# Optimization experiments

Hardware: AMD Instinct MI355X
Metric: run time of the kernel (lower is better)

The kernel has to match this reference:

```python
import jax, jax.numpy as jnp
import numpy as np

N, D_IN, HID, OUT, E = 131072, 256, 1024, 1, 100


def setup_inputs() -> dict:
    key = jax.random.key(0)
    k = jax.random.split(key, 7)
    return {
        "x": jax.random.normal(k[0], (N, D_IN), dtype=jnp.float32),
        "W1": jax.random.normal(k[1], (HID, D_IN), dtype=jnp.float32) * 0.05,
        "b1": jax.random.normal(k[2], (HID,), dtype=jnp.float32) * 0.05,
        "We": jax.random.normal(k[3], (E, OUT, HID), dtype=jnp.float32) * 0.05,
        "be": jax.random.normal(k[4], (E, OUT), dtype=jnp.float32) * 0.05,
        "num": jax.random.randint(k[5], (N,), 0, E, dtype=jnp.int64),
        "c": jax.random.randint(k[6], (E,), 0, E, dtype=jnp.int64),
    }


def reference(x, W1, b1, We, be, num, c):
    # feature: Linear + ReLU  -> [N, HID]
    h = jax.nn.relu(x @ W1.T + b1)
    # per-sample expert index: c[num[i]]
    e = c[num]                                  # [N]
    Wg = We[e]                                  # [N, OUT, HID] gathered expert weights
    bg = be[e]                                  # [N, OUT]
    y = jnp.einsum('noh,nh->no', Wg, h) + bg    # per-sample expert linear
    return jax.nn.sigmoid(y)
```

## Files before the change

kernel.cpp:

```cpp
#include <hip/hip_runtime.h>
#include <stdint.h>

#define N_SAMP 131072
#define DIN    256
#define HIDN   1024
#define BROWS  128
#define NTHREADS 256
#define NCHUNK 16

typedef __attribute__((ext_vector_type(8))) short short8;
typedef __attribute__((ext_vector_type(4))) float f32x4;

__device__ __forceinline__ unsigned short f2bf(float f) {
  unsigned u = __float_as_uint(f);
  u += 0x7fffu + ((u >> 16) & 1u);
  return (unsigned short)(u >> 16);
}

__device__ __forceinline__ short8 pack8(float4 a, float4 b) {
  short8 r;
  r[0] = (short)f2bf(a.x); r[1] = (short)f2bf(a.y);
  r[2] = (short)f2bf(a.z); r[3] = (short)f2bf(a.w);
  r[4] = (short)f2bf(b.x); r[5] = (short)f2bf(b.y);
  r[6] = (short)f2bf(b.z); r[7] = (short)f2bf(b.w);
  return r;
}

__global__ __launch_bounds__(256) void w1_pack(const float* __restrict__ W1,
                                               unsigned short* __restrict__ o) {
  int idx = blockIdx.x * 256 + threadIdx.x;
  int l  = idx & 63;
  int nt = (idx >> 6) & 3;
  int s  = (idx >> 8) & 7;
  int ch = idx >> 11;
  int col = ch * 64 + nt * 16 + (l & 15);
  int k0  = s * 32 + (l >> 4) * 8;
  const float* src = W1 + (size_t)col * DIN + k0;
  float4 f0 = *(const float4*)src;
  float4 f1 = *(const float4*)(src + 4);
  ((short8*)o)[idx] = pack8(f0, f1);
}

template <bool WBF>
__global__ __launch_bounds__(NTHREADS, 2) void fused_kernel(
    const float* __restrict__ x,
    const float* __restrict__ W1f,
    const unsigned short* __restrict__ W1p,
    const float* __restrict__ b1,
    const float* __restrict__ We,
    const float* __restrict__ be,
    const int* __restrict__ num,
    const int* __restrict__ c,
    float* __restrict__ out)
{
  __shared__ int e_sh[BROWS];

  const int tid  = threadIdx.x;
  const int lane = tid & 63;
  const int w    = tid >> 6;
  const int n    = lane & 15;
  const int quad = lane >> 4;
  const int R0   = blockIdx.x * BROWS;

  if (tid < BROWS) e_sh[tid] = c[num[R0 + tid]];

  short8 afr[2][8];
  {
    const float* xr0 = x + (size_t)(R0 + w * 32 + n) * DIN + quad * 8;
#pragma unroll
    for (int t = 0; t < 2; ++t) {
      const float* xr = xr0 + (size_t)t * 16 * DIN;
#pragma unroll
      for (int s = 0; s < 8; ++s) {
        float4 f0 = *(const float4*)(xr + s * 32);
        float4 f1 = *(const float4*)(xr + s * 32 + 4);
        afr[t][s] = pack8(f0, f1);
      }
    }
  }

  __syncthreads();

  int eoff[2][4];
#pragma unroll
  for (int t = 0; t < 2; ++t)
#pragma unroll
    for (int r = 0; r < 4; ++r)
      eoff[t][r] = e_sh[w * 32 + t * 16 + quad * 4 + r] * HIDN;

  float yacc[2][4] = {{0.f, 0.f, 0.f, 0.f}, {0.f, 0.f, 0.f, 0.f}};

  const int lane8 = lane * 8;

  for (int ch = 0; ch < NCHUNK; ++ch) {
    f32x4 acc[2][4];
#pragma unroll
    for (int t = 0; t < 2; ++t)
#pragma unroll
      for (int nt = 0; nt < 4; ++nt)
        acc[t][nt] = (f32x4){0.f, 0.f, 0.f, 0.f};

    if (WBF) {
      const unsigned short* Wpc = W1p + (size_t)ch * 16384;
      short8 bfr[2][4];
      {
        const unsigned short* bp = Wpc + lane8;
#pragma unroll
        for (int nt = 0; nt < 4; ++nt)
          bfr[0][nt] = *(const short8*)(bp + nt * 512);
      }
#pragma unroll
      for (int s = 0; s < 8; ++s) {
        if (s + 1 < 8) {
          const unsigned short* bp = Wpc + (s + 1) * 2048 + lane8;
#pragma unroll
          for (int nt = 0; nt < 4; ++nt)
            bfr[(s + 1) & 1][nt] = *(const short8*)(bp + nt * 512);
        }
#pragma unroll
        for (int t = 0; t < 2; ++t)
#pragma unroll
          for (int nt = 0; nt < 4; ++nt)
            acc[t][nt] = __builtin_amdgcn_mfma_f32_16x16x32_bf16(
                afr[t][s], bfr[s & 1][nt], acc[t][nt], 0, 0, 0);
      }
    } else {
#pragma unroll
      for (int s = 0; s < 8; ++s) {
        short8 bfr[4];
#pragma unroll
        for (int nt = 0; nt < 4; ++nt) {
          int col = ch * 64 + nt * 16 + n;
          const float* gs = W1f + (size_t)col * DIN + s * 32 + quad * 8;
          float4 f0 = *(const float4*)gs;
          float4 f1 = *(const float4*)(gs + 4);
          bfr[nt] = pack8(f0, f1);
        }
#pragma unroll
        for (int t = 0; t < 2; ++t)
#pragma unroll
          for (int nt = 0; nt < 4; ++nt)
            acc[t][nt] = __builtin_amdgcn_mfma_f32_16x16x32_bf16(
                afr[t][s], bfr[nt], acc[t][nt], 0, 0, 0);
      }
    }

#pragma unroll
    for (int nt = 0; nt < 4; ++nt) {
      int col = ch * 64 + nt * 16 + n;
      float bv = b1[col];
      const float* Wec = We + col;
#pragma unroll
      for (int t = 0; t < 2; ++t)
#pragma unroll
        for (int r = 0; r < 4; ++r) {
          float h = acc[t][nt][r] + bv;
          h = fmaxf(h, 0.f);
          yacc[t][r] = fmaf(h, Wec[eoff[t][r]], yacc[t][r]);
        }
    }
  }

#pragma unroll
  for (int t = 0; t < 2; ++t)
#pragma unroll
    for (int r = 0; r < 4; ++r) {
      float v = yacc[t][r];
      v += __shfl_xor(v, 1);
      v += __shfl_xor(v, 2);
      v += __shfl_xor(v, 4);
      v += __shfl_xor(v, 8);
      yacc[t][r] = v;
    }

  if (n == 0) {
#pragma unroll
    for (int t = 0; t < 2; ++t)
#pragma unroll
      for (int r = 0; r < 4; ++r) {
        int row = R0 + w * 32 + t * 16 + quad * 4 + r;
        float yy = yacc[t][r] + be[eoff[t][r] >> 10];
        out[row] = 1.f / (1.f + __expf(-yy));
      }
  }
}

extern "C" void kernel_launch(void* const* d_in, const int* in_sizes, int n_in,
                              void* d_out, int out_size, void* d_ws, size_t ws_size,
                              hipStream_t stream) {
  const float* x   = (const float*)d_in[0];
  const float* W1  = (const float*)d_in[1];
  const float* b1  = (const float*)d_in[2];
  const float* We  = (const float*)d_in[3];
  const float* be  = (const float*)d_in[4];
  const int*   num = (const int*)d_in[5];
  const int*   c   = (const int*)d_in[6];
  float* out = (float*)d_out;

  const size_t w1p_bytes = (size_t)HIDN * DIN * sizeof(unsigned short);
  const bool usebf = ws_size >= w1p_bytes;
  unsigned short* w1p = (unsigned short*)d_ws;

  if (usebf) {
    w1_pack<<<dim3((HIDN * DIN / 8) / 256), dim3(256), 0, stream>>>(W1, w1p);
    fused_kernel<true><<<dim3(N_SAMP / BROWS), dim3(NTHREADS), 0, stream>>>(
        x, W1, w1p, b1, We, be, num, c, out);
  } else {
    fused_kernel<false><<<dim3(N_SAMP / BROWS), dim3(NTHREADS), 0, stream>>>(
        x, W1, w1p, b1, We, be, num, c, out);
  }
}
```

Before: 306.3 us.

## Stage W1 chunks in double-buffered LDS via async global-to-LDS loads

```diff
diff --git a/kernel.cpp b/kernel.cpp
--- a/kernel.cpp
+++ b/kernel.cpp
@@ -53,6 +53,7 @@
     const int* __restrict__ c,
     float* __restrict__ out)
 {
+  __shared__ unsigned short Wt[2][16384];
   __shared__ int e_sh[BROWS];
 
   const int tid  = threadIdx.x;
@@ -79,6 +80,31 @@
     }
   }
 
+  if (WBF) {
+#pragma unroll
+    for (int j = 0; j < 8; ++j) {
+      int inst = w * 8 + j;
+      const unsigned short* g = W1p + inst * 512 + lane * 8;
+      __builtin_amdgcn_global_load_lds(
+          (const __attribute__((address_space(1))) unsigned int*)g,
+          (__attribute__((address_space(3))) unsigned int*)(&Wt[0][0] + inst * 512),
+          16, 0, 0);
+    }
+  } else {
+#pragma unroll
+    for (int j = 0; j < 8; ++j) {
+      int id = tid + j * NTHREADS;
+      int l = id & 63, f = id >> 6;
+      int nt = f & 3, s = f >> 2;
+      int col = nt * 16 + (l & 15);
+      int k0  = s * 32 + (l >> 4) * 8;
+      const float* gs = W1f + (size_t)col * DIN + k0;
+      float4 f0 = *(const float4*)gs;
+      float4 f1 = *(const float4*)(gs + 4);
+      *(short8*)&Wt[0][f * 512 + l * 8] = pack8(f0, f1);
+    }
+  }
+
   __syncthreads();
 
   int eoff[2][4];
@@ -90,9 +116,39 @@
 
   float yacc[2][4] = {{0.f, 0.f, 0.f, 0.f}, {0.f, 0.f, 0.f, 0.f}};
 
-  const int lane8 = lane * 8;
-
+  int buf = 0;
   for (int ch = 0; ch < NCHUNK; ++ch) {
+    if (ch + 1 < NCHUNK) {
+      if (WBF) {
+        const unsigned short* Wg = W1p + (size_t)(ch + 1) * 16384;
+        unsigned short* db = &Wt[buf ^ 1][0];
+#pragma unroll
+        for (int j = 0; j < 8; ++j) {
+          int inst = w * 8 + j;
+          const unsigned short* g = Wg + inst * 512 + lane * 8;
+          __builtin_amdgcn_global_load_lds(
+              (const __attribute__((address_space(1))) unsigned int*)g,
+              (__attribute__((address_space(3))) unsigned int*)(db + inst * 512),
+              16, 0, 0);
+        }
+      } else {
+        const float* Wc = W1f + (size_t)(ch + 1) * 64 * DIN;
+#pragma unroll
+        for (int j = 0; j < 8; ++j) {
+          int id = tid + j * NTHREADS;
+          int l = id & 63, f = id >> 6;
+          int nt = f & 3, s = f >> 2;
+          int col = nt * 16 + (l & 15);
+          int k0  = s * 32 + (l >> 4) * 8;
+          const float* gs = Wc + (size_t)col * DIN + k0;
+          float4 f0 = *(const float4*)gs;
+          float4 f1 = *(const float4*)(gs + 4);
+          *(short8*)&Wt[buf ^ 1][f * 512 + l * 8] = pack8(f0, f1);
+        }
+      }
+    }
+
+    const char* Bbase = (const char*)&Wt[buf][0] + lane * 16;
     f32x4 acc[2][4];
 #pragma unroll
     for (int t = 0; t < 2; ++t)
@@ -100,49 +156,18 @@
       for (int nt = 0; nt < 4; ++nt)
         acc[t][nt] = (f32x4){0.f, 0.f, 0.f, 0.f};
 
-    if (WBF) {
-      const unsigned short* Wpc = W1p + (size_t)ch * 16384;
-      short8 bfr[2][4];
-      {
-        const unsigned short* bp = Wpc + lane8;
+#pragma unroll
+    for (int s = 0; s < 8; ++s) {
+      short8 bfr[4];
+#pragma unroll
+      for (int nt = 0; nt < 4; ++nt)
+        bfr[nt] = *(const short8*)(Bbase + (s * 4 + nt) * 1024);
+#pragma unroll
+      for (int t = 0; t < 2; ++t)
 #pragma unroll
         for (int nt = 0; nt < 4; ++nt)
-          bfr[0][nt] = *(const short8*)(bp + nt * 512);
-      }
-#pragma unroll
-      for (int s = 0; s < 8; ++s) {
-        if (s + 1 < 8) {
-          const unsigned short* bp = Wpc + (s + 1) * 2048 + lane8;
-#pragma unroll
-          for (int nt = 0; nt < 4; ++nt)
-            bfr[(s + 1) & 1][nt] = *(const short8*)(bp + nt * 512);
-        }
-#pragma unroll
-        for (int t = 0; t < 2; ++t)
-#pragma unroll
-          for (int nt = 0; nt < 4; ++nt)
-            acc[t][nt] = __builtin_amdgcn_mfma_f32_16x16x32_bf16(
-                afr[t][s], bfr[s & 1][nt], acc[t][nt], 0, 0, 0);
-      }
-    } else {
-#pragma unroll
-      for (int s = 0; s < 8; ++s) {
-        short8 bfr[4];
-#pragma unroll
-        for (int nt = 0; nt < 4; ++nt) {
-          int col = ch * 64 + nt * 16 + n;
-          const float* gs = W1f + (size_t)col * DIN + s * 32 + quad * 8;
-          float4 f0 = *(const float4*)gs;
-          float4 f1 = *(const float4*)(gs + 4);
-          bfr[nt] = pack8(f0, f1);
-        }
-#pragma unroll
-        for (int t = 0; t < 2; ++t)
-#pragma unroll
-          for (int nt = 0; nt < 4; ++nt)
-            acc[t][nt] = __builtin_amdgcn_mfma_f32_16x16x32_bf16(
-                afr[t][s], bfr[nt], acc[t][nt], 0, 0, 0);
-      }
+          acc[t][nt] = __builtin_amdgcn_mfma_f32_16x16x32_bf16(
+              afr[t][s], bfr[nt], acc[t][nt], 0, 0, 0);
     }
 
 #pragma unroll
@@ -159,6 +184,9 @@
           yacc[t][r] = fmaf(h, Wec[eoff[t][r]], yacc[t][r]);
         }
     }
+
+    __syncthreads();
+    buf ^= 1;
   }
 
 #pragma unroll
```

New measurement: 261.4 us. 1.17x faster.
